# Performance work log

Hardware: AMD Instinct MI355X
Metric: run time of the kernel (lower is better)

## Reference

```python
import jax, jax.numpy as jnp
import numpy as np
import math

B, N, D = 8, 2048, 64


def setup_inputs() -> dict:
    key = jax.random.key(0)
    kq, kk, kv, kd = jax.random.split(key, 4)
    Q = jax.random.normal(kq, (B, N, D), dtype=jnp.float32)
    K = jax.random.normal(kk, (B, N, D), dtype=jnp.float32)
    V = jax.random.normal(kv, (B, N, D), dtype=jnp.float32)
    dist_matrix = jax.random.uniform(kd, (N, N), dtype=jnp.float32)
    return {"Q": Q, "K": K, "V": V, "dist_matrix": dist_matrix}


def rescale_distance_matrix(dist_matrix):
    # (1 + e^1) / (1 + exp(1 - dist))
    c = 1.0
    return (c + math.e) / (c + jnp.exp(c - dist_matrix))


def reference(Q, K, V, dist_matrix):
    d_k = K.shape[-1]
    inv_sqrt_dk = 1.0 / math.sqrt(d_k)
    # [B, N, N] raw attention logits
    qk = jnp.einsum("bnd,bmd->bnm", Q, K)
    # ReLU then multiply by rescaled distance matrix [N, N] on the right
    scores = jnp.matmul(jax.nn.relu(qk), rescale_distance_matrix(dist_matrix)) * inv_sqrt_dk
    attn = jax.nn.softmax(scores, axis=-1)
    context = jnp.einsum("bnm,bmd->bnd", attn, V)
    return context
```

## Files before the change

kernel.cpp:

```cpp
#include <hip/hip_runtime.h>


typedef _Float16 f16;
typedef _Float16 f16x8 __attribute__((ext_vector_type(8)));
typedef float    f32x4 __attribute__((ext_vector_type(4)));

#define AS1C(p) ((const __attribute__((address_space(1))) void*)(p))
#define AS3(p)  ((__attribute__((address_space(3))) void*)(p))

__device__ __forceinline__ f16x8 cvt_f16x8(float4 a, float4 b){
  f16x8 v;
  v[0]=(f16)a.x; v[1]=(f16)a.y; v[2]=(f16)a.z; v[3]=(f16)a.w;
  v[4]=(f16)b.x; v[5]=(f16)b.y; v[6]=(f16)b.z; v[7]=(f16)b.w;
  return v;
}

__launch_bounds__(256, 2)
__global__ void k_qk(const float* __restrict__ Q, const float* __restrict__ Km,
                     const float* __restrict__ V, const float* __restrict__ Dm,
                     f16* __restrict__ Ph, f16* __restrict__ RhT,
                     f16* __restrict__ VhT){
  __shared__ __align__(16) char shm[36864];
  const int bid = blockIdx.x;
  const int t = threadIdx.x;

  if (bid >= 2048){
    f16* tl = (f16*)shm;
    const int c = t & 63, g = t >> 6;
    if (bid < 3072){
      const int pid = bid - 2048;
      const int k0 = (pid & 31)*64, m0 = (pid >> 5)*64;
#pragma unroll
      for (int i=0;i<16;++i){
        int k = g*16 + i;
        float d = Dm[(size_t)(k0 + k)*2048 + m0 + c];
        tl[k*65 + c] = (f16)(3.7182818284590452f / (1.0f + __expf(1.0f - d)));
      }
      __syncthreads();
#pragma unroll
      for (int i=0;i<16;++i){
        int m = g*16 + i;
        RhT[(size_t)(m0 + m)*2048 + k0 + c] = tl[c*65 + m];
      }
    } else {
      const int pid = bid - 3072;
      const int m0 = (pid & 31)*64, b = pid >> 5;
#pragma unroll
      for (int i=0;i<16;++i){
        int m = g*16 + i;
        tl[m*65 + c] = (f16)V[((size_t)b*2048 + m0 + m)*64 + c];
      }
      __syncthreads();
#pragma unroll
      for (int i=0;i<16;++i){
        int d = g*16 + i;
        VhT[((size_t)b*64 + d)*2048 + m0 + c] = tl[c*65 + d];
      }
    }
    return;
  }

  f16* Qt = (f16*)shm;
  f16* Kt = (f16*)(shm + 18432);
  f16* Tt = (f16*)shm;

  const int w = t>>6, l = t&63, lr = l&15, q = l>>4;
  const int m0 = (bid & 15)*128, n0 = ((bid>>4) & 15)*128, b = bid >> 8;
  const int wr = (w>>1)*64, wc = (w&1)*64;
  const float* Qb = Q  + ((size_t)b*2048 + n0)*64;
  const float* Kb = Km + ((size_t)b*2048 + m0)*64;

  const int sr = t>>3, sc = t&7;
#pragma unroll
  for (int j=0;j<4;++j){
    int row = sr + 32*j;
    const float* p  = Qb + (size_t)row*64 + sc*8;
    *(f16x8*)(Qt + row*72 + sc*8) = cvt_f16x8(*(const float4*)p, *(const float4*)(p+4));
    const float* pk = Kb + (size_t)row*64 + sc*8;
    *(f16x8*)(Kt + row*72 + sc*8) = cvt_f16x8(*(const float4*)pk, *(const float4*)(pk+4));
  }
  __syncthreads();

  f32x4 acc[4][4] = {};
#pragma unroll
  for (int kc=0;kc<2;++kc){
    f16x8 af[4], bf[4];
#pragma unroll
    for (int ti=0;ti<4;++ti) af[ti] = *(const f16x8*)(Qt + (wr+16*ti+lr)*72 + kc*32 + q*8);
#pragma unroll
    for (int tj=0;tj<4;++tj) bf[tj] = *(const f16x8*)(Kt + (wc+16*tj+lr)*72 + kc*32 + q*8);
#pragma unroll
    for (int ti=0;ti<4;++ti)
#pragma unroll
      for (int tj=0;tj<4;++tj)
        acc[ti][tj] = __builtin_amdgcn_mfma_f32_16x16x32_f16(af[ti], bf[tj], acc[ti][tj], 0,0,0);
  }
  __syncthreads();
#pragma unroll
  for (int ti=0;ti<4;++ti)
#pragma unroll
    for (int tj=0;tj<4;++tj)
#pragma unroll
      for (int r=0;r<4;++r)
        Tt[(wr+16*ti+4*q+r)*136 + wc+16*tj+lr] = (f16)(fmaxf(acc[ti][tj][r],0.f)*0.125f);
  __syncthreads();
  const int g16 = t&15, r0 = t>>4;
#pragma unroll
  for (int j=0;j<8;++j){
    int row = r0 + 16*j;
    *(f16x8*)(Ph + ((size_t)b*2048 + n0 + row)*2048 + m0 + g16*8) =
        *(const f16x8*)(Tt + row*136 + g16*8);
  }
}

__launch_bounds__(256, 2)
__global__ void k_attn(const f16* __restrict__ Ph, const f16* __restrict__ RhT,
                       const f16* __restrict__ VhT, f16* __restrict__ Op,
                       float* __restrict__ mp, float* __restrict__ lp){
  __shared__ __align__(16) char smem[49152];
  f16*  Pbuf = (f16*)smem;
  f16*  Rbuf = (f16*)(smem + 16384);
  f16*  El   = (f16*)smem;
  float* stat_max = (float*)(smem + 33792);
  float* stat_sum = (float*)(smem + 34816);

  const int t = threadIdx.x, w = t>>6, l = t&63, lr = l&15, q = l>>4;
  const int bid = blockIdx.x;
  const int b = bid & 7, jq = (bid >> 3) & 7, nb = bid >> 6;
  const int n0 = nb*128, jg = jq*256;
  const int wc = w*64;

  const f16* Pblk = Ph  + ((size_t)b*2048 + n0)*2048;
  const f16* Vb   = VhT + (size_t)b*64*2048;

  const f16* srcP[2];
  const f16* srcR[4];
#pragma unroll
  for (int i=0;i<2;++i){
    int slot = i*256 + t, row = slot>>2, g = slot&3;
    srcP[i] = Pblk + (size_t)row*2048 + (g ^ ((row>>1)&3))*8;
  }
#pragma unroll
  for (int i=0;i<4;++i){
    int slot = i*256 + t, row = slot>>2, g = slot&3;
    srcR[i] = RhT + (size_t)(jg + row)*2048 + (g ^ ((row>>1)&3))*8;
  }

  auto stage = [&](int kc){
    const int cb = kc & 1, k0 = kc*32;
#pragma unroll
    for (int i=0;i<2;++i)
      __builtin_amdgcn_global_load_lds(AS1C(srcP[i] + k0),
                                       AS3(Pbuf + cb*4096 + i*2048 + w*512), 16, 0, 0);
#pragma unroll
    for (int i=0;i<4;++i)
      __builtin_amdgcn_global_load_lds(AS1C(srcR[i] + k0),
                                       AS3(Rbuf + cb*8192 + i*2048 + w*512), 16, 0, 0);
  };

  const int swz = (lr>>1)&3;
  f32x4 acc[8][4] = {};
  f32x4 Oacc[2][2][2] = {};

  stage(0);
#pragma unroll 2
  for (int kc = 0; kc < 64; ++kc){
    __syncthreads();
    if (kc < 63) stage(kc+1);
    const int cb = kc & 1;
    const f16* Pb = Pbuf + cb*4096;
    const f16* Rb = Rbuf + cb*8192;
    f16x8 bf[4];
#pragma unroll
    for (int tj=0;tj<4;++tj)
      bf[tj] = *(const f16x8*)(Rb + (wc + 16*tj + lr)*32 + (q ^ swz)*8);
#pragma unroll
    for (int ti=0;ti<8;++ti){
      f16x8 af = *(const f16x8*)(Pb + (16*ti + lr)*32 + (q ^ swz)*8);
#pragma unroll
      for (int tj=0;tj<4;++tj)
        acc[ti][tj] = __builtin_amdgcn_mfma_f32_16x16x32_f16(af, bf[tj], acc[ti][tj], 0,0,0);
    }
  }
  __syncthreads();

#pragma unroll
  for (int p=0;p<2;++p){
    float pm[4][4];
#pragma unroll
    for (int ti=0;ti<4;++ti)
#pragma unroll
      for (int r=0;r<4;++r)
        pm[ti][r] = fmaxf(fmaxf(acc[4*p+ti][0][r], acc[4*p+ti][1][r]),
                          fmaxf(acc[4*p+ti][2][r], acc[4*p+ti][3][r]));
#pragma unroll
    for (int mm=1;mm<16;mm<<=1)
#pragma unroll
      for (int ti=0;ti<4;++ti)
#pragma unroll
        for (int r=0;r<4;++r)
          pm[ti][r] = fmaxf(pm[ti][r], __shfl_xor(pm[ti][r], mm));
    if (lr == 0)
#pragma unroll
      for (int ti=0;ti<4;++ti)
#pragma unroll
        for (int r=0;r<4;++r)
          stat_max[(16*ti + 4*q + r)*4 + w] = pm[ti][r];
    __syncthreads();

    float Mn[4][4], ps[4][4];
#pragma unroll
    for (int ti=0;ti<4;++ti)
#pragma unroll
      for (int r=0;r<4;++r){
        int row = 16*ti + 4*q + r;
        float4 s4 = *(const float4*)&stat_max[row*4];
        Mn[ti][r] = fmaxf(fmaxf(s4.x,s4.y), fmaxf(s4.z,s4.w));
        ps[ti][r] = 0.f;
      }
#pragma unroll
    for (int ti=0;ti<4;++ti)
#pragma unroll
      for (int tj=0;tj<4;++tj)
#pragma unroll
        for (int r=0;r<4;++r){
          float e = __expf(acc[4*p+ti][tj][r] - Mn[ti][r]);
          ps[ti][r] += e;
          El[(16*ti + 4*q + r)*264 + wc + 16*tj + lr] = (f16)e;
        }
#pragma unroll
    for (int mm=1;mm<16;mm<<=1)
#pragma unroll
      for (int ti=0;ti<4;++ti)
#pragma unroll
        for (int r=0;r<4;++r)
          ps[ti][r] += __shfl_xor(ps[ti][r], mm);
    if (lr == 0)
#pragma unroll
      for (int ti=0;ti<4;++ti)
#pragma unroll
        for (int r=0;r<4;++r)
          stat_sum[(16*ti + 4*q + r)*4 + w] = ps[ti][r];
    __syncthreads();

    if (w == 0 && lr == 0)
#pragma unroll
      for (int ti=0;ti<4;++ti)
#pragma unroll
        for (int r=0;r<4;++r){
          int row = 16*ti + 4*q + r;
          float4 s4 = *(const float4*)&stat_sum[row*4];
          mp[bid*128 + 64*p + row] = Mn[ti][r];
          lp[bid*128 + 64*p + row] = s4.x + s4.y + s4.z + s4.w;
        }

    const int erb = 32*(w&1), vcb = 32*(w>>1);
#pragma unroll
    for (int ks=0; ks<8; ++ks){
      f16x8 ae[2], bv[2];
#pragma unroll
      for (int a=0;a<2;++a)
        ae[a] = *(const f16x8*)(El + (erb + 16*a + lr)*264 + ks*32 + q*8);
#pragma unroll
      for (int bb=0;bb<2;++bb)
        bv[bb] = *(const f16x8*)(Vb + (size_t)(vcb + 16*bb + lr)*2048 + jg + ks*32 + q*8);
#pragma unroll
      for (int a=0;a<2;++a)
#pragma unroll
        for (int bb=0;bb<2;++bb)
          Oacc[p][a][bb] = __builtin_amdgcn_mfma_f32_16x16x32_f16(ae[a], bv[bb], Oacc[p][a][bb], 0,0,0);
    }
    __syncthreads();
  }

#pragma unroll
  for (int p=0;p<2;++p)
#pragma unroll
    for (int a=0;a<2;++a)
#pragma unroll
      for (int bb=0;bb<2;++bb)
#pragma unroll
        for (int r=0;r<4;++r){
          int row = 64*p + 32*(w&1) + 16*a + 4*q + r;
          int col = 32*(w>>1) + 16*bb + lr;
          Op[((size_t)bid*128 + row)*64 + col] = (f16)Oacc[p][a][bb][r];
        }
}

__global__ void k_comb(const f16* __restrict__ Op, const float* __restrict__ mp,
                       const float* __restrict__ lp, float* __restrict__ out){
  const int rb = blockIdx.x >> 2;
  const int qr = blockIdx.x & 3;
  const int b = rb & 7, nb = rb >> 3;
  const int pb = nb*64 + b;
  const int t = threadIdx.x;
  const int row = qr*32 + (t >> 3);
  const int c0 = (t & 7)*8;

  float m_[8], a_[8];
  float M = -1e30f, den = 0.f;
#pragma unroll
  for (int i=0;i<8;++i){ m_[i] = mp[(pb + i*8)*128 + row]; M = fmaxf(M, m_[i]); }
#pragma unroll
  for (int i=0;i<8;++i){ a_[i] = __expf(m_[i] - M); den += a_[i]*lp[(pb + i*8)*128 + row]; }
  float inv = 1.0f / den;

  float o[8] = {};
#pragma unroll
  for (int i=0;i<8;++i){
    f16x8 v = *(const f16x8*)(Op + ((size_t)(pb + i*8)*128 + row)*64 + c0);
#pragma unroll
    for (int e=0;e<8;++e) o[e] += a_[i]*(float)v[e];
  }
  float4 o0, o1;
  o0.x=o[0]*inv; o0.y=o[1]*inv; o0.z=o[2]*inv; o0.w=o[3]*inv;
  o1.x=o[4]*inv; o1.y=o[5]*inv; o1.z=o[6]*inv; o1.w=o[7]*inv;
  float* dst = out + ((size_t)b*2048 + nb*128 + row)*64 + c0;
  *(float4*)dst = o0;
  *(float4*)(dst+4) = o1;
}

extern "C" void kernel_launch(void* const* d_in, const int* in_sizes, int n_in,
                              void* d_out, int out_size, void* d_ws, size_t ws_size,
                              hipStream_t stream){
  (void)in_sizes; (void)n_in; (void)out_size; (void)ws_size;
  const float* Q  = (const float*)d_in[0];
  const float* K  = (const float*)d_in[1];
  const float* V  = (const float*)d_in[2];
  const float* Dm = (const float*)d_in[3];
  float* out = (float*)d_out;
  char* ws = (char*)d_ws;
  f16* Ph  = (f16*)ws;
  f16* RhT = (f16*)(ws + (size_t)64*1024*1024);
  f16* VhT = (f16*)(ws + (size_t)72*1024*1024);
  f16* Op  = (f16*)(ws + (size_t)74*1024*1024);
  float* mpp = (float*)(ws + (size_t)90*1024*1024);
  float* lpp = mpp + 1024*128;

  k_qk   <<<dim3(3328), 256, 0, stream>>>(Q, K, V, Dm, Ph, RhT, VhT);
  k_attn <<<dim3(1024), 256, 0, stream>>>(Ph, RhT, VhT, Op, mpp, lpp);
  k_comb <<<dim3(512),  256, 0, stream>>>(Op, mpp, lpp, out);
}
```

Baseline: 236.1 us.

## Load R operand straight to registers and pipeline the k-loop with manual waits

The R (rescaled distance) tile is no longer staged through LDS. Each wave loads its own B-fragments directly from global memory into registers, double-buffered across a manually unrolled two-step loop. The generic __syncthreads is replaced by s_waitcnt vmcnt plus s_barrier, so only the P-tile LDS copies are waited on before each step. This cuts LDS traffic and the shared-memory footprint, in exchange for global loads that are less coalesced (16-byte pieces spread across many 4 KB-strided rows) and hand-tuned wait counts that are fragile.

Result: slower. 261.5 us (+10.7%).

```diff
diff --git a/kernel.cpp b/kernel.cpp
--- a/kernel.cpp
+++ b/kernel.cpp
@@ -117,9 +117,8 @@
 __global__ void k_attn(const f16* __restrict__ Ph, const f16* __restrict__ RhT,
                        const f16* __restrict__ VhT, f16* __restrict__ Op,
                        float* __restrict__ mp, float* __restrict__ lp){
-  __shared__ __align__(16) char smem[49152];
+  __shared__ __align__(16) char smem[35840];
   f16*  Pbuf = (f16*)smem;
-  f16*  Rbuf = (f16*)(smem + 16384);
   f16*  El   = (f16*)smem;
   float* stat_max = (float*)(smem + 33792);
   float* stat_sum = (float*)(smem + 34816);
@@ -134,17 +133,15 @@
   const f16* Vb   = VhT + (size_t)b*64*2048;
 
   const f16* srcP[2];
-  const f16* srcR[4];
 #pragma unroll
   for (int i=0;i<2;++i){
     int slot = i*256 + t, row = slot>>2, g = slot&3;
     srcP[i] = Pblk + (size_t)row*2048 + (g ^ ((row>>1)&3))*8;
   }
-#pragma unroll
-  for (int i=0;i<4;++i){
-    int slot = i*256 + t, row = slot>>2, g = slot&3;
-    srcR[i] = RhT + (size_t)(jg + row)*2048 + (g ^ ((row>>1)&3))*8;
-  }
+  const f16* Rrow[4];
+#pragma unroll
+  for (int tj=0;tj<4;++tj)
+    Rrow[tj] = RhT + (size_t)(jg + wc + 16*tj + lr)*2048 + q*8;
 
   auto stage = [&](int kc){
     const int cb = kc & 1, k0 = kc*32;
@@ -152,34 +149,53 @@
     for (int i=0;i<2;++i)
       __builtin_amdgcn_global_load_lds(AS1C(srcP[i] + k0),
                                        AS3(Pbuf + cb*4096 + i*2048 + w*512), 16, 0, 0);
-#pragma unroll
-    for (int i=0;i<4;++i)
-      __builtin_amdgcn_global_load_lds(AS1C(srcR[i] + k0),
-                                       AS3(Rbuf + cb*8192 + i*2048 + w*512), 16, 0, 0);
   };
 
   const int swz = (lr>>1)&3;
   f32x4 acc[8][4] = {};
   f32x4 Oacc[2][2][2] = {};
 
+  f16x8 bf0[4], bf1[4];
   stage(0);
-#pragma unroll 2
-  for (int kc = 0; kc < 64; ++kc){
-    __syncthreads();
+#pragma unroll
+  for (int tj=0;tj<4;++tj) bf0[tj] = *(const f16x8*)(Rrow[tj]);
+
+  for (int kc = 0; kc < 64; kc += 2){
+    asm volatile("s_waitcnt vmcnt(4)" ::: "memory");
+    __builtin_amdgcn_s_barrier();
+    __builtin_amdgcn_sched_barrier(0);
     if (kc < 63) stage(kc+1);
-    const int cb = kc & 1;
-    const f16* Pb = Pbuf + cb*4096;
-    const f16* Rb = Rbuf + cb*8192;
-    f16x8 bf[4];
-#pragma unroll
-    for (int tj=0;tj<4;++tj)
-      bf[tj] = *(const f16x8*)(Rb + (wc + 16*tj + lr)*32 + (q ^ swz)*8);
-#pragma unroll
-    for (int ti=0;ti<8;++ti){
-      f16x8 af = *(const f16x8*)(Pb + (16*ti + lr)*32 + (q ^ swz)*8);
+    if (kc < 63)
 #pragma unroll
       for (int tj=0;tj<4;++tj)
-        acc[ti][tj] = __builtin_amdgcn_mfma_f32_16x16x32_f16(af, bf[tj], acc[ti][tj], 0,0,0);
+        bf1[tj] = *(const f16x8*)(Rrow[tj] + (kc+1)*32);
+    {
+      const f16* Pb = Pbuf;
+#pragma unroll
+      for (int ti=0;ti<8;++ti){
+        f16x8 af = *(const f16x8*)(Pb + (16*ti + lr)*32 + (q ^ swz)*8);
+#pragma unroll
+        for (int tj=0;tj<4;++tj)
+          acc[ti][tj] = __builtin_amdgcn_mfma_f32_16x16x32_f16(af, bf0[tj], acc[ti][tj], 0,0,0);
+      }
+    }
+    asm volatile("s_waitcnt vmcnt(4)" ::: "memory");
+    __builtin_amdgcn_s_barrier();
+    __builtin_amdgcn_sched_barrier(0);
+    if (kc+1 < 63) stage(kc+2);
+    if (kc+1 < 63)
+#pragma unroll
+      for (int tj=0;tj<4;++tj)
+        bf0[tj] = *(const f16x8*)(Rrow[tj] + (kc+2)*32);
+    {
+      const f16* Pb = Pbuf + 4096;
+#pragma unroll
+      for (int ti=0;ti<8;++ti){
+        f16x8 af = *(const f16x8*)(Pb + (16*ti + lr)*32 + (q ^ swz)*8);
+#pragma unroll
+        for (int tj=0;tj<4;++tj)
+          acc[ti][tj] = __builtin_amdgcn_mfma_f32_16x16x32_f16(af, bf1[tj], acc[ti][tj], 0,0,0);
+      }
     }
   }
   __syncthreads();
```
